# Kernel optimization log

Measured on AMD Instinct MI355X. Metric: run time of the kernel, lower is better.

Reference implementation:

```python
import jax, jax.numpy as jnp
import numpy as np

S = 384    # size2d (s = 128*3)
D1 = 3     # lattice dimension+1 (hardcoded d=d1=3 in the module)

# canonical simplex offsets built exactly as in __init__:
# start [[0,1,2]]*3, then canonical[-1:,1]=-2, canonical[-2:,2]=-1
CANONICAL = jnp.array([[0, 1, 2],
                       [0, 1, -1],
                       [0, -2, -1]], dtype=jnp.int32)


def setup_inputs() -> dict:
    key = jax.random.key(0)
    k1, k2, k3 = jax.random.split(key, 3)
    B, N = 64, 8192
    # get_model passes x[:, :3] * (s // 2); emulate unit-cube points scaled by 192
    pc1 = (jax.random.uniform(k1, (B, 3, N), jnp.float32) * 2.0 - 1.0) * (S // 2)
    features = jax.random.normal(k2, (B, 3, N), jnp.float32)
    tm = jax.random.normal(k3, (B, 3, 3), jnp.float32)
    # F.normalize(trans_matrix, dim=1)
    trans_mat = tm / jnp.maximum(jnp.linalg.norm(tm, axis=1, keepdims=True), 1e-12)
    return {"pc1": pc1, "features": features, "trans_mat": trans_mat}


def reference(pc1, features, trans_mat):
    B, _, N = pc1.shape
    # ---- get_keys_and_barycentric ----
    elevated = jnp.einsum('bij,bjn->bin', trans_mat, pc1)          # [B,3,N]
    greedy = jnp.round(elevated / D1) * D1
    el_minus_gr = elevated - greedy
    # rank = inverse permutation of descending argsort along lattice axis
    idx = jnp.argsort(-el_minus_gr, axis=1)
    rank = jnp.argsort(idx, axis=1).astype(jnp.int32)              # [B,3,N]
    remainder_sum = jnp.sum(greedy, axis=1, keepdims=True) / D1    # [B,1,N] (exact ints)
    rank_f = rank.astype(jnp.float32)
    cond = ((rank_f >= D1 - remainder_sum) & (remainder_sum > 0)) | \
           ((rank_f < -remainder_sum) & (remainder_sum < 0))
    sign = jnp.where(remainder_sum > 0, -1.0, 0.0) + jnp.where(remainder_sum < 0, 1.0, 0.0)
    shift = D1 * sign * cond.astype(jnp.float32)                   # [B,3,N]
    greedy = greedy + shift
    rank = rank + shift.astype(jnp.int32) + remainder_sum.astype(jnp.int32)
    greedy_i = greedy.astype(jnp.int32)
    # NOTE: in the torch source the two non-accumulating index-assigns
    # (barycentric[b, 3-rank, n] += E then barycentric[b, 3-rank, n] -= E,
    # with self.d == self.d1 == 3) write to identical index sets and cancel
    # exactly; after the final `+= 1.0 + barycentric[:, d1]` the barycentric
    # weights are 1 on lattice channel 0 and 0 elsewhere. Reproduce faithfully.
    barycentric = jnp.zeros((B, D1, N), pc1.dtype).at[:, 0, :].set(1.0)
    keys = greedy_i[:, :, :, None] + CANONICAL[rank]               # [B,3,N,3]

    # ---- splat into dense 2D grid ----
    coord = keys[:, :2].reshape(B, 2, D1 * N)                      # [B,2,3N]
    offset = coord.min(axis=2)                                     # [B,2]
    coord = coord - offset[:, :, None]
    tmp = barycentric[:, None, :, :] * features[:, :, None, :]     # [B,3feat,3lat,N]
    tmp = jnp.transpose(tmp, (0, 1, 3, 2)).reshape(B, 3, D1 * N)   # [B,3,3N]
    tmp = jnp.transpose(tmp, (0, 2, 1))                            # [B,3N,3]
    pts_pick = (-offset) % D1                                      # [B,2]
    oob = coord >= S                                               # [B,2,3N]
    coord = jnp.where(oob, 0, coord)
    tmp = jnp.where(oob.any(axis=1)[:, :, None], 0.0, tmp)
    bidx = jnp.arange(B)[:, None]
    # sparse_coo.to_dense() accumulates duplicate coords -> scatter-add
    splatted = jnp.zeros((B, S, S, 3), pc1.dtype).at[bidx, coord[:, 0], coord[:, 1]].add(tmp)
    # filter_2d[i] = splatted[i, pp0::3, pp1::3][:S//3, :S//3]
    base = jnp.arange(S // D1) * D1                                # [128]
    rows = pts_pick[:, 0:1] + base[None, :]                        # [B,128]
    cols = pts_pick[:, 1:2] + base[None, :]
    filt = jax.vmap(lambda sp, r, c: sp[r][:, c])(splatted, rows, cols)  # [B,128,128,3]
    return filt
```

## Files before the change

### kernel.cpp

```cpp
#include <hip/hip_runtime.h>
#include <math.h>

#define NB     64
#define NPTS   8192
#define S2D    384
#define GW     128
#define QROWS  32
#define BLK    1024
#define PPT    8
#define ACCN   (QROWS * GW * 3)

__global__ __launch_bounds__(1024) void fused_splat(const float* __restrict__ pc1,
                                                    const float* __restrict__ feat,
                                                    const float* __restrict__ tm,
                                                    float* __restrict__ out) {
    const int b   = blockIdx.x >> 2;
    const int q   = blockIdx.x & 3;
    const int tid = threadIdx.x;

    __shared__ __align__(16) float acc[ACCN];
    __shared__ int s_off[2];

    if (tid < 2) s_off[tid] = 0x7FFFFFFF;
#pragma unroll
    for (int i = 0; i < ACCN / BLK; i++)
        acc[tid + i * BLK] = 0.0f;

    float t[9];
#pragma unroll
    for (int i = 0; i < 9; i++) t[i] = tm[b * 9 + i];

    const float4* __restrict__ pc4 = (const float4*)(pc1  + (size_t)b * 3 * NPTS);
    const float4* __restrict__ ft4 = (const float4*)(feat + (size_t)b * 3 * NPTS);

    float p0[PPT], p1[PPT], p2[PPT], f0[PPT], f1[PPT], f2[PPT];
#pragma unroll
    for (int k = 0; k < 2; k++) {
        const int base = k * 1024 + tid;
        ((float4*)p0)[k] = pc4[0 * 2048 + base];
        ((float4*)p1)[k] = pc4[1 * 2048 + base];
        ((float4*)p2)[k] = pc4[2 * 2048 + base];
        ((float4*)f0)[k] = ft4[0 * 2048 + base];
        ((float4*)f1)[k] = ft4[1 * 2048 + base];
        ((float4*)f2)[k] = ft4[2 * 2048 + base];
    }

    int gi0[PPT], gi1[PPT];
    int m0 = 0x7FFFFFFF, m1 = 0x7FFFFFFF;

#pragma unroll
    for (int j = 0; j < PPT; j++) {
        float g[3], v[3];
#pragma unroll
        for (int i = 0; i < 3; i++) {
            float e  = fmaf(t[i*3+2], p2[j], fmaf(t[i*3+1], p1[j], t[i*3+0] * p0[j]));
            float qq = __fdiv_rn(e, 3.0f);
            g[i] = rintf(qq) * 3.0f;
            v[i] = e - g[i];
        }

        int rank[3];
#pragma unroll
        for (int i = 0; i < 3; i++) {
            int r = 0;
#pragma unroll
            for (int jj = 0; jj < 3; jj++)
                if (v[jj] > v[i] || (v[jj] == v[i] && jj < i)) r++;
            rank[i] = r;
        }

        const float rs_f = __fdiv_rn(g[0] + g[1] + g[2], 3.0f);
        const int   rs   = (int)rs_f;

#pragma unroll
        for (int i = 0; i < 2; i++) {
            const float rank_f = (float)rank[i];
            const bool cond = ((rank_f >= 3.0f - rs_f) && (rs_f > 0.0f)) ||
                              ((rank_f <  -rs_f)       && (rs_f < 0.0f));
            const float sign  = (rs_f > 0.0f ? -1.0f : 0.0f) + (rs_f < 0.0f ? 1.0f : 0.0f);
            const float shift = 3.0f * sign * (cond ? 1.0f : 0.0f);
            const int gi = (int)(g[i] + shift);
            const int rfin = rank[i] + (int)shift + rs;
            const int cand = gi - min(max(rfin, 0), 2);
            if (i == 0) { gi0[j] = gi; m0 = min(m0, cand); }
            else        { gi1[j] = gi; m1 = min(m1, cand); }
        }
    }

#pragma unroll
    for (int off = 32; off > 0; off >>= 1) {
        m0 = min(m0, __shfl_down(m0, off));
        m1 = min(m1, __shfl_down(m1, off));
    }
    if ((tid & 63) == 0) {
        atomicMin(&s_off[0], m0);
        atomicMin(&s_off[1], m1);
    }
    __syncthreads();

    const int off0 = s_off[0], off1 = s_off[1];
    const int pp0 = ((-off0) % 3 + 3) % 3;
    const int pp1 = ((-off1) % 3 + 3) % 3;
    const int rlo = q * QROWS, rhi = rlo + QROWS;

#pragma unroll
    for (int j = 0; j < PPT; j++) {
        const int c0 = gi0[j] - off0;
        const int c1 = gi1[j] - off1;
        if (c0 < S2D && c1 < S2D) {
            const int i0 = (c0 - pp0) / 3;
            if (i0 >= rlo && i0 < rhi) {
                const int j0 = (c1 - pp1) / 3;
                float* dst = acc + (((i0 - rlo) * GW) + j0) * 3;
                atomicAdd(dst + 0, f0[j]);
                atomicAdd(dst + 1, f1[j]);
                atomicAdd(dst + 2, f2[j]);
            }
        }
    }
    __syncthreads();

    float4* __restrict__ dst4 = (float4*)(out + ((size_t)b * GW + rlo) * GW * 3);
    const float4* __restrict__ src4 = (const float4*)acc;
#pragma unroll
    for (int i = 0; i < ACCN / (4 * BLK); i++)
        dst4[tid + i * BLK] = src4[tid + i * BLK];
}

extern "C" void kernel_launch(void* const* d_in, const int* in_sizes, int n_in,
                              void* d_out, int out_size, void* d_ws, size_t ws_size,
                              hipStream_t stream) {
    const float* pc1  = (const float*)d_in[0];
    const float* feat = (const float*)d_in[1];
    const float* tm   = (const float*)d_in[2];
    float* out = (float*)d_out;

    fused_splat<<<NB * 4, BLK, 0, stream>>>(pc1, feat, tm, out);
}
```

Measured before the change: 94.73 us.

## Split lattice computation into separate kernel to avoid redundant per-quarter recompute

The fused kernel recomputed the lattice keys for every point in each of the four row-quarter blocks per batch. The change moves that computation into its own kernel, which runs once per point and writes packed integer coordinates plus a clamped rank to workspace. The splat kernel then reads these packed ints instead of recomputing. This adds a second launch and a workspace round-trip in exchange for removing four-fold redundant arithmetic.

Result: slower. 97.11 us (+2.5%).

```diff
diff --git a/kernel.cpp b/kernel.cpp
--- a/kernel.cpp
+++ b/kernel.cpp
@@ -6,14 +6,74 @@
 #define S2D    384
 #define GW     128
 #define QROWS  32
-#define BLK    1024
-#define PPT    8
+#define BLK2   1024
 #define ACCN   (QROWS * GW * 3)
 
-__global__ __launch_bounds__(1024) void fused_splat(const float* __restrict__ pc1,
-                                                    const float* __restrict__ feat,
-                                                    const float* __restrict__ tm,
-                                                    float* __restrict__ out) {
+__global__ __launch_bounds__(256) void lattice_kernel(const float* __restrict__ pc1,
+                                                      const float* __restrict__ tm,
+                                                      int* __restrict__ ws0,
+                                                      int* __restrict__ ws1) {
+    const int b     = blockIdx.y;
+    const int base4 = blockIdx.x * 256 + threadIdx.x;
+
+    float t[9];
+#pragma unroll
+    for (int i = 0; i < 9; i++) t[i] = tm[b * 9 + i];
+
+    const float4* __restrict__ pc4 = (const float4*)(pc1 + (size_t)b * 3 * NPTS);
+    const float4 P0 = pc4[0 * 2048 + base4];
+    const float4 P1 = pc4[1 * 2048 + base4];
+    const float4 P2 = pc4[2 * 2048 + base4];
+    const float* p0 = (const float*)&P0;
+    const float* p1 = (const float*)&P1;
+    const float* p2 = (const float*)&P2;
+
+    int4 pk0, pk1;
+    int* o0 = (int*)&pk0;
+    int* o1 = (int*)&pk1;
+
+#pragma unroll
+    for (int e = 0; e < 4; e++) {
+        float g[3], v[3];
+#pragma unroll
+        for (int i = 0; i < 3; i++) {
+            float ev = fmaf(t[i*3+2], p2[e], fmaf(t[i*3+1], p1[e], t[i*3+0] * p0[e]));
+            float qq = __fdiv_rn(ev, 3.0f);
+            g[i] = rintf(qq) * 3.0f;
+            v[i] = ev - g[i];
+        }
+        int rank[3];
+#pragma unroll
+        for (int i = 0; i < 3; i++) {
+            int r = 0;
+#pragma unroll
+            for (int j = 0; j < 3; j++)
+                if (v[j] > v[i] || (v[j] == v[i] && j < i)) r++;
+            rank[i] = r;
+        }
+        const float rs_f = __fdiv_rn(g[0] + g[1] + g[2], 3.0f);
+        const int   rs   = (int)rs_f;
+#pragma unroll
+        for (int i = 0; i < 2; i++) {
+            const float rank_f = (float)rank[i];
+            const bool cond = ((rank_f >= 3.0f - rs_f) && (rs_f > 0.0f)) ||
+                              ((rank_f <  -rs_f)       && (rs_f < 0.0f));
+            const float sign  = (rs_f > 0.0f ? -1.0f : 0.0f) + (rs_f < 0.0f ? 1.0f : 0.0f);
+            const float shift = 3.0f * sign * (cond ? 1.0f : 0.0f);
+            const int gi  = (int)(g[i] + shift);
+            const int cl  = min(max(rank[i] + (int)shift + rs, 0), 2);
+            const int pk  = gi * 4 + cl;
+            if (i == 0) o0[e] = pk; else o1[e] = pk;
+        }
+    }
+    ((int4*)(ws0 + (size_t)b * NPTS))[base4] = pk0;
+    ((int4*)(ws1 + (size_t)b * NPTS))[base4] = pk1;
+}
+
+__global__ __launch_bounds__(1024) void splat_kernel(const int* __restrict__ ws0,
+                                                     const int* __restrict__ ws1,
+                                                     const float* __restrict__ feat,
+                                                     float* __restrict__ out) {
     const int b   = blockIdx.x >> 2;
     const int q   = blockIdx.x & 3;
     const int tid = threadIdx.x;
@@ -22,71 +82,33 @@
     __shared__ int s_off[2];
 
     if (tid < 2) s_off[tid] = 0x7FFFFFFF;
-#pragma unroll
-    for (int i = 0; i < ACCN / BLK; i++)
-        acc[tid + i * BLK] = 0.0f;
 
-    float t[9];
-#pragma unroll
-    for (int i = 0; i < 9; i++) t[i] = tm[b * 9 + i];
-
-    const float4* __restrict__ pc4 = (const float4*)(pc1  + (size_t)b * 3 * NPTS);
+    const int4*   __restrict__ w04 = (const int4*)(ws0 + (size_t)b * NPTS);
+    const int4*   __restrict__ w14 = (const int4*)(ws1 + (size_t)b * NPTS);
     const float4* __restrict__ ft4 = (const float4*)(feat + (size_t)b * 3 * NPTS);
 
-    float p0[PPT], p1[PPT], p2[PPT], f0[PPT], f1[PPT], f2[PPT];
+    int pk0[8], pk1[8];
+    float f0[8], f1[8], f2[8];
 #pragma unroll
     for (int k = 0; k < 2; k++) {
         const int base = k * 1024 + tid;
-        ((float4*)p0)[k] = pc4[0 * 2048 + base];
-        ((float4*)p1)[k] = pc4[1 * 2048 + base];
-        ((float4*)p2)[k] = pc4[2 * 2048 + base];
-        ((float4*)f0)[k] = ft4[0 * 2048 + base];
-        ((float4*)f1)[k] = ft4[1 * 2048 + base];
-        ((float4*)f2)[k] = ft4[2 * 2048 + base];
+        ((int4*)pk0)[k]   = w04[base];
+        ((int4*)pk1)[k]   = w14[base];
+        ((float4*)f0)[k]  = ft4[0 * 2048 + base];
+        ((float4*)f1)[k]  = ft4[1 * 2048 + base];
+        ((float4*)f2)[k]  = ft4[2 * 2048 + base];
     }
 
-    int gi0[PPT], gi1[PPT];
+#pragma unroll
+    for (int i = 0; i < ACCN / BLK2; i++)
+        acc[tid + i * BLK2] = 0.0f;
+
     int m0 = 0x7FFFFFFF, m1 = 0x7FFFFFFF;
-
 #pragma unroll
-    for (int j = 0; j < PPT; j++) {
-        float g[3], v[3];
-#pragma unroll
-        for (int i = 0; i < 3; i++) {
-            float e  = fmaf(t[i*3+2], p2[j], fmaf(t[i*3+1], p1[j], t[i*3+0] * p0[j]));
-            float qq = __fdiv_rn(e, 3.0f);
-            g[i] = rintf(qq) * 3.0f;
-            v[i] = e - g[i];
-        }
-
-        int rank[3];
-#pragma unroll
-        for (int i = 0; i < 3; i++) {
-            int r = 0;
-#pragma unroll
-            for (int jj = 0; jj < 3; jj++)
-                if (v[jj] > v[i] || (v[jj] == v[i] && jj < i)) r++;
-            rank[i] = r;
-        }
-
-        const float rs_f = __fdiv_rn(g[0] + g[1] + g[2], 3.0f);
-        const int   rs   = (int)rs_f;
-
-#pragma unroll
-        for (int i = 0; i < 2; i++) {
-            const float rank_f = (float)rank[i];
-            const bool cond = ((rank_f >= 3.0f - rs_f) && (rs_f > 0.0f)) ||
-                              ((rank_f <  -rs_f)       && (rs_f < 0.0f));
-            const float sign  = (rs_f > 0.0f ? -1.0f : 0.0f) + (rs_f < 0.0f ? 1.0f : 0.0f);
-            const float shift = 3.0f * sign * (cond ? 1.0f : 0.0f);
-            const int gi = (int)(g[i] + shift);
-            const int rfin = rank[i] + (int)shift + rs;
-            const int cand = gi - min(max(rfin, 0), 2);
-            if (i == 0) { gi0[j] = gi; m0 = min(m0, cand); }
-            else        { gi1[j] = gi; m1 = min(m1, cand); }
-        }
+    for (int j = 0; j < 8; j++) {
+        m0 = min(m0, (pk0[j] >> 2) - (pk0[j] & 3));
+        m1 = min(m1, (pk1[j] >> 2) - (pk1[j] & 3));
     }
-
 #pragma unroll
     for (int off = 32; off > 0; off >>= 1) {
         m0 = min(m0, __shfl_down(m0, off));
@@ -104,13 +126,13 @@
     const int rlo = q * QROWS, rhi = rlo + QROWS;
 
 #pragma unroll
-    for (int j = 0; j < PPT; j++) {
-        const int c0 = gi0[j] - off0;
-        const int c1 = gi1[j] - off1;
+    for (int j = 0; j < 8; j++) {
+        const int c0 = (pk0[j] >> 2) - off0;
+        const int c1 = (pk1[j] >> 2) - off1;
         if (c0 < S2D && c1 < S2D) {
-            const int i0 = (c0 - pp0) / 3;
+            const int i0 = (unsigned)(c0 - pp0) / 3u;
             if (i0 >= rlo && i0 < rhi) {
-                const int j0 = (c1 - pp1) / 3;
+                const int j0 = (unsigned)(c1 - pp1) / 3u;
                 float* dst = acc + (((i0 - rlo) * GW) + j0) * 3;
                 atomicAdd(dst + 0, f0[j]);
                 atomicAdd(dst + 1, f1[j]);
@@ -123,8 +145,8 @@
     float4* __restrict__ dst4 = (float4*)(out + ((size_t)b * GW + rlo) * GW * 3);
     const float4* __restrict__ src4 = (const float4*)acc;
 #pragma unroll
-    for (int i = 0; i < ACCN / (4 * BLK); i++)
-        dst4[tid + i * BLK] = src4[tid + i * BLK];
+    for (int i = 0; i < ACCN / (4 * BLK2); i++)
+        dst4[tid + i * BLK2] = src4[tid + i * BLK2];
 }
 
 extern "C" void kernel_launch(void* const* d_in, const int* in_sizes, int n_in,
@@ -134,6 +156,10 @@
     const float* feat = (const float*)d_in[1];
     const float* tm   = (const float*)d_in[2];
     float* out = (float*)d_out;
+    int* ws0 = (int*)d_ws;
+    int* ws1 = ws0 + (size_t)NB * NPTS;
 
-    fused_splat<<<NB * 4, BLK, 0, stream>>>(pc1, feat, tm, out);
+    dim3 g1(NPTS / (256 * 4), NB);
+    lattice_kernel<<<g1, 256, 0, stream>>>(pc1, tm, ws0, ws1);
+    splat_kernel<<<NB * 4, BLK2, 0, stream>>>(ws0, ws1, feat, out);
 }
```
